# Performance work log

Hardware: AMD Instinct MI355X
Metric: run time of the kernel (lower is better)

The kernel has to match this reference:

```python
import jax, jax.numpy as jnp
import numpy as np

B, N, D = 8, 1024, 64
NUM_FEAT = 11
FEATURE_PARAM = 1.0   # threshold used by feature_masking2
NEG_INF = -1e9        # finite stand-in for masked_fill(-inf)


def setup_inputs() -> dict:
    key = jax.random.key(0)
    k1, k2, k3 = jax.random.split(key, 3)
    x = jax.random.normal(k1, (B, N, D), dtype=jnp.float32)
    # lengths in [1, N] so no row is fully padded
    x_lengths = jax.random.randint(k2, (B,), 1, N + 1)
    # nn.Parameter initialized to zeros would trivialize the op; use small randn
    feature_importance = 0.1 * jax.random.normal(k3, (NUM_FEAT,), dtype=jnp.float32)
    return {"x": x, "x_lengths": x_lengths, "feature_importance": feature_importance}


def reference(x, x_lengths, feature_importance):
    xf = x[:, :, :NUM_FEAT]                                   # [B,N,11]
    # pairwise weighted L1 distance -> [B,N,N]
    fd = jnp.abs(xf[:, :, None, :] - xf[:, None, :, :])       # [B,N,N,11]
    attn = jnp.sum(fd * feature_importance, axis=-1)          # [B,N,N]
    # feature_masking2: keep pairs whose weighted distance is below threshold,
    # convert distance to similarity by negation
    mask = (attn < FEATURE_PARAM).astype(attn.dtype)
    attn = -attn * mask
    # global_masking: mask padded key positions per sequence length
    valid = jnp.arange(N)[None, :] < x_lengths[:, None]       # [B,N]
    attn = jnp.where(valid[:, None, :], attn, NEG_INF)
    attn = jax.nn.softmax(attn, axis=-1)
    attn = jnp.where(jnp.isnan(attn), 0.0, attn)
    return attn
```

## Files before the change

### kernel.cpp

```cpp
#include <hip/hip_runtime.h>

#define NN 1024
#define DD 64
#define NF 11
#define TI 16
#define BT 1024

__global__ __launch_bounds__(BT, 8) void featuresim_kernel(
    const float* __restrict__ x,
    const int* __restrict__ x_lengths,
    const float* __restrict__ fimp,
    float* __restrict__ out)
{
    const int tid = threadIdx.x;
    const int b   = blockIdx.x >> 6;
    const int i0  = (blockIdx.x & 63) * TI;
    const int len = x_lengths[b];

    float fi[NF];
    #pragma unroll
    for (int k = 0; k < NF; ++k) fi[k] = fimp[k];

    const int j0 = tid;
    float fj[NF];
    {
        const float4* p = reinterpret_cast<const float4*>(
            x + (size_t)(b * NN + j0) * DD);
        float4 a = p[0], c = p[1], d = p[2];
        fj[0] = a.x; fj[1] = a.y; fj[2]  = a.z; fj[3] = a.w;
        fj[4] = c.x; fj[5] = c.y; fj[6]  = c.z; fj[7] = c.w;
        fj[8] = d.x; fj[9] = d.y; fj[10] = d.z;
    }
    const bool valid = j0 < len;

    __shared__ float partials[TI][BT];
    __shared__ float totals[TI];

    float e[TI];

    #pragma unroll
    for (int r = 0; r < TI; ++r) {
        const float* qp = x + (size_t)(b * NN + i0 + r) * DD;
        float q[NF];
        #pragma unroll
        for (int k = 0; k < NF; ++k) q[k] = qp[k];

        float s = 0.0f;
        #pragma unroll
        for (int k = 0; k < NF; ++k) {
            float d = q[k] - fj[k];
            s = fmaf(-fabsf(d), fi[k], s);
        }
        float val = (s > -1.0f) ? s : 0.0f;
        float ev  = valid ? __expf(val) : 0.0f;
        e[r] = ev;
        partials[r][tid] = ev;
    }
    __syncthreads();

    const int lane = tid & 63;
    const int wid  = tid >> 6;
    {
        float s = 0.0f;
        #pragma unroll
        for (int m = 0; m < BT / 64; ++m)
            s += partials[wid][lane + 64 * m];
        #pragma unroll
        for (int off = 32; off >= 1; off >>= 1)
            s += __shfl_xor(s, off, 64);
        if (lane == 0) totals[wid] = s;
    }
    __syncthreads();

    #pragma unroll
    for (int r = 0; r < TI; ++r) {
        const float inv = __builtin_amdgcn_rcpf(totals[r]);
        out[(size_t)(b * NN + i0 + r) * NN + j0] = e[r] * inv;
    }
}

extern "C" void kernel_launch(void* const* d_in, const int* in_sizes, int n_in,
                              void* d_out, int out_size, void* d_ws, size_t ws_size,
                              hipStream_t stream) {
    const float* x    = (const float*)d_in[0];
    const int*   xlen = (const int*)d_in[1];
    const float* fimp = (const float*)d_in[2];
    float*       out  = (float*)d_out;

    const int B = in_sizes[1];
    dim3 grid(B * (NN / TI));
    dim3 block(BT);
    featuresim_kernel<<<grid, block, 0, stream>>>(x, xlen, fimp, out);
}
```

Measured before the change: 19.21 us.

## Split row softmax into two halves to overlap reduction with compute

```diff
diff --git a/kernel.cpp b/kernel.cpp
--- a/kernel.cpp
+++ b/kernel.cpp
@@ -4,6 +4,7 @@
 #define DD 64
 #define NF 11
 #define TI 16
+#define H  8
 #define BT 1024
 
 __global__ __launch_bounds__(BT, 8) void featuresim_kernel(
@@ -38,42 +39,58 @@
 
     float e[TI];
 
+    const int lane = tid & 63;
+    const int wid  = tid >> 6;
+
+    #define ROW_COMPUTE(r)                                                  \
+    {                                                                       \
+        const float* qp = x + (size_t)(b * NN + i0 + (r)) * DD;             \
+        float s = 0.0f;                                                     \
+        _Pragma("unroll")                                                   \
+        for (int k = 0; k < NF; ++k) {                                      \
+            float d = qp[k] - fj[k];                                        \
+            s = fmaf(-fabsf(d), fi[k], s);                                  \
+        }                                                                   \
+        float val = (s > -1.0f) ? s : 0.0f;                                 \
+        float ev  = valid ? __expf(val) : 0.0f;                             \
+        e[r] = ev;                                                          \
+        partials[r][tid] = ev;                                              \
+    }
+
+    #define ROW_REDUCE(r)                                                   \
+    {                                                                       \
+        float s = 0.0f;                                                     \
+        _Pragma("unroll")                                                   \
+        for (int m = 0; m < 4; ++m) {                                       \
+            float4 v4 = *reinterpret_cast<const float4*>(                   \
+                &partials[r][lane * 4 + 256 * m]);                          \
+            s += (v4.x + v4.y) + (v4.z + v4.w);                             \
+        }                                                                   \
+        _Pragma("unroll")                                                   \
+        for (int off = 32; off >= 1; off >>= 1)                             \
+            s += __shfl_xor(s, off, 64);                                    \
+        if (lane == 0) totals[r] = s;                                       \
+    }
+
     #pragma unroll
-    for (int r = 0; r < TI; ++r) {
-        const float* qp = x + (size_t)(b * NN + i0 + r) * DD;
-        float q[NF];
-        #pragma unroll
-        for (int k = 0; k < NF; ++k) q[k] = qp[k];
-
-        float s = 0.0f;
-        #pragma unroll
-        for (int k = 0; k < NF; ++k) {
-            float d = q[k] - fj[k];
-            s = fmaf(-fabsf(d), fi[k], s);
-        }
-        float val = (s > -1.0f) ? s : 0.0f;
-        float ev  = valid ? __expf(val) : 0.0f;
-        e[r] = ev;
-        partials[r][tid] = ev;
-    }
+    for (int r = 0; r < H; ++r) ROW_COMPUTE(r)
     __syncthreads();
 
-    const int lane = tid & 63;
-    const int wid  = tid >> 6;
-    {
-        float s = 0.0f;
-        #pragma unroll
-        for (int m = 0; m < BT / 64; ++m)
-            s += partials[wid][lane + 64 * m];
-        #pragma unroll
-        for (int off = 32; off >= 1; off >>= 1)
-            s += __shfl_xor(s, off, 64);
-        if (lane == 0) totals[wid] = s;
+    if (wid < H) ROW_REDUCE(wid)
+    #pragma unroll
+    for (int r = H; r < TI; ++r) ROW_COMPUTE(r)
+    __syncthreads();
+
+    if (wid >= H) ROW_REDUCE(H + (wid - H))
+    #pragma unroll
+    for (int r = 0; r < H; ++r) {
+        const float inv = __builtin_amdgcn_rcpf(totals[r]);
+        out[(size_t)(b * NN + i0 + r) * NN + j0] = e[r] * inv;
     }
     __syncthreads();
 
     #pragma unroll
-    for (int r = 0; r < TI; ++r) {
+    for (int r = H; r < TI; ++r) {
         const float inv = __builtin_amdgcn_rcpf(totals[r]);
         out[(size_t)(b * NN + i0 + r) * NN + j0] = e[r] * inv;
     }
```

Result: no change. 19.18 us (-0.2%).

## Process query rows in groups of four to interleave reductions with stores

Applied to the files above, without the earlier changes.

```diff
diff --git a/kernel.cpp b/kernel.cpp
--- a/kernel.cpp
+++ b/kernel.cpp
@@ -4,6 +4,8 @@
 #define DD 64
 #define NF 11
 #define TI 16
+#define G  4
+#define NG (TI / G)
 #define BT 1024
 
 __global__ __launch_bounds__(BT, 8) void featuresim_kernel(
@@ -21,61 +23,66 @@
     #pragma unroll
     for (int k = 0; k < NF; ++k) fi[k] = fimp[k];
 
-    const int j0 = tid;
     float fj[NF];
     {
         const float4* p = reinterpret_cast<const float4*>(
-            x + (size_t)(b * NN + j0) * DD);
+            x + (size_t)(b * NN + tid) * DD);
         float4 a = p[0], c = p[1], d = p[2];
         fj[0] = a.x; fj[1] = a.y; fj[2]  = a.z; fj[3] = a.w;
         fj[4] = c.x; fj[5] = c.y; fj[6]  = c.z; fj[7] = c.w;
         fj[8] = d.x; fj[9] = d.y; fj[10] = d.z;
     }
-    const bool valid = j0 < len;
+    const bool valid = tid < len;
 
-    __shared__ float partials[TI][BT];
-    __shared__ float totals[TI];
-
-    float e[TI];
-
-    #pragma unroll
-    for (int r = 0; r < TI; ++r) {
-        const float* qp = x + (size_t)(b * NN + i0 + r) * DD;
-        float q[NF];
-        #pragma unroll
-        for (int k = 0; k < NF; ++k) q[k] = qp[k];
-
-        float s = 0.0f;
-        #pragma unroll
-        for (int k = 0; k < NF; ++k) {
-            float d = q[k] - fj[k];
-            s = fmaf(-fabsf(d), fi[k], s);
-        }
-        float val = (s > -1.0f) ? s : 0.0f;
-        float ev  = valid ? __expf(val) : 0.0f;
-        e[r] = ev;
-        partials[r][tid] = ev;
-    }
-    __syncthreads();
+    __shared__ float partials[G][BT];
+    __shared__ float totals[G];
 
     const int lane = tid & 63;
     const int wid  = tid >> 6;
-    {
-        float s = 0.0f;
-        #pragma unroll
-        for (int m = 0; m < BT / 64; ++m)
-            s += partials[wid][lane + 64 * m];
-        #pragma unroll
-        for (int off = 32; off >= 1; off >>= 1)
-            s += __shfl_xor(s, off, 64);
-        if (lane == 0) totals[wid] = s;
-    }
-    __syncthreads();
 
     #pragma unroll
-    for (int r = 0; r < TI; ++r) {
-        const float inv = __builtin_amdgcn_rcpf(totals[r]);
-        out[(size_t)(b * NN + i0 + r) * NN + j0] = e[r] * inv;
+    for (int g = 0; g < NG; ++g) {
+        float eg[G];
+        #pragma unroll
+        for (int rr = 0; rr < G; ++rr) {
+            const int r = g * G + rr;
+            const float* qp = x + (size_t)(b * NN + i0 + r) * DD;
+            float s = 0.0f;
+            #pragma unroll
+            for (int k = 0; k < NF; ++k) {
+                float d = qp[k] - fj[k];
+                s = fmaf(-fabsf(d), fi[k], s);
+            }
+            float val = (s > -1.0f) ? s : 0.0f;
+            eg[rr] = valid ? __expf(val) : 0.0f;
+            partials[rr][tid] = eg[rr];
+        }
+        asm volatile("s_waitcnt lgkmcnt(0)" ::: "memory");
+        __builtin_amdgcn_s_barrier();
+
+        if ((wid >> 2) == g) {
+            const int rr = wid & 3;
+            float s = 0.0f;
+            #pragma unroll
+            for (int m = 0; m < 4; ++m) {
+                float4 v4 = *reinterpret_cast<const float4*>(
+                    &partials[rr][lane * 4 + 256 * m]);
+                s += (v4.x + v4.y) + (v4.z + v4.w);
+            }
+            #pragma unroll
+            for (int off = 32; off >= 1; off >>= 1)
+                s += __shfl_xor(s, off, 64);
+            if (lane == 0) totals[rr] = s;
+        }
+        asm volatile("s_waitcnt lgkmcnt(0)" ::: "memory");
+        __builtin_amdgcn_s_barrier();
+
+        #pragma unroll
+        for (int rr = 0; rr < G; ++rr) {
+            const int r = g * G + rr;
+            const float inv = __builtin_amdgcn_rcpf(totals[rr]);
+            out[(size_t)(b * NN + i0 + r) * NN + tid] = eg[rr] * inv;
+        }
     }
 }
 
```

Measured after the change: 20.78 us. 1.08x slower.
